# Kernel optimization log

Measured on AMD Instinct MI355X. Metric: run time of the kernel, lower is better.

## Reference

```python
import jax, jax.numpy as jnp
import numpy as np

B, L, D, H = 16, 1024, 1024, 16
HD = D // H  # head dim = 64


def setup_inputs() -> dict:
    rng = jax.random.key(0)
    ks = jax.random.split(rng, 12)
    s = 0.02
    return {
        "key": jax.random.normal(ks[0], (B, L, D), jnp.float32),
        "value": jax.random.normal(ks[1], (B, L, D), jnp.float32),
        "query": jax.random.normal(ks[2], (B, L, D), jnp.float32),
        "atten_masks": jax.random.randint(ks[3], (B, L, L), 0, 2, jnp.int32),
        "Wk": jax.random.normal(ks[4], (D, D), jnp.float32) * s,
        "bk": jnp.zeros((D,), jnp.float32),
        "Wq": jax.random.normal(ks[5], (D, D), jnp.float32) * s,
        "bq": jnp.zeros((D,), jnp.float32),
        "Wv": jax.random.normal(ks[6], (D, D), jnp.float32) * s,
        "bv": jnp.zeros((D,), jnp.float32),
        "Wp": jax.random.normal(ks[7], (D, D), jnp.float32) * s,
        "bp": jnp.zeros((D,), jnp.float32),
    }


def reference(key, value, query, atten_masks, Wk, bk, Wq, bq, Wv, bv, Wp, bp):
    # Linear projections (torch nn.Linear: x @ W^T + b)
    def lin(x, W, b):
        return x @ W.T + b

    # [B, L, D] -> [B, H, L, HD]
    def heads(x):
        return x.reshape(B, L, H, HD).transpose(0, 2, 1, 3)

    k = heads(lin(key, Wk, bk))
    q = heads(lin(query, Wq, bq))
    v = heads(lin(value, Wv, bv))

    scale = 1.0 / np.sqrt(HD).astype(np.float32)
    att = jnp.einsum("bhqd,bhkd->bhqk", q, k) * scale  # [B, H, L, L]
    att = jnp.where(atten_masks[:, None, :, :] == 0, -jnp.inf, att)
    att = jax.nn.softmax(att, axis=-1)

    y = jnp.einsum("bhqk,bhkd->bhqd", att, v)  # [B, H, L, HD]
    y = y.transpose(0, 2, 1, 3).reshape(B, L, D)
    return lin(y, Wp, bp)
```

## Files before the change

kernel.cpp:

```cpp
#include <hip/hip_runtime.h>

typedef __bf16 bf16_t;
typedef __bf16 bf16x4 __attribute__((ext_vector_type(4)));
typedef __bf16 bf16x8 __attribute__((ext_vector_type(8)));
typedef float f32x4 __attribute__((ext_vector_type(4)));
typedef float f32x16 __attribute__((ext_vector_type(16)));
typedef unsigned u32x2 __attribute__((ext_vector_type(2)));

#define QSCALE 0.18033688f

__device__ __forceinline__ int swz(int row) { return (row ^ (row >> 3)) & 7; }
__device__ __forceinline__ int swz2(int row) { return (row ^ (row >> 2)) & 3; }
__device__ __forceinline__ int swzv(int row) { return (row ^ (row >> 3)) & 15; }

__device__ __forceinline__ f32x4 mfma16(bf16x8 a, bf16x8 b, f32x4 c) {
  return __builtin_amdgcn_mfma_f32_16x16x32_bf16(a, b, c, 0, 0, 0);
}
__device__ __forceinline__ f32x16 mfma32(bf16x8 a, bf16x8 b, f32x16 c) {
  return __builtin_amdgcn_mfma_f32_32x32x16_bf16(a, b, c, 0, 0, 0);
}

__device__ __forceinline__ void gl_lds16(const void* g, void* l) {
  __builtin_amdgcn_global_load_lds(
      (const __attribute__((address_space(1))) unsigned int*)g,
      (__attribute__((address_space(3))) unsigned int*)l, 16, 0, 0);
}

__global__ __launch_bounds__(256) void cvt_all_kernel(
    const float* __restrict__ key, const float* __restrict__ query,
    const float* __restrict__ value, const float* __restrict__ Wk,
    const float* __restrict__ Wq, const float* __restrict__ Wv,
    const float* __restrict__ Wp, const int* __restrict__ mask,
    bf16_t* __restrict__ I1, bf16_t* __restrict__ I2, bf16_t* __restrict__ I3,
    bf16_t* __restrict__ Wkb, bf16_t* __restrict__ Wqb,
    bf16_t* __restrict__ Wvb, bf16_t* __restrict__ Wpb,
    unsigned* __restrict__ mbits) {
  const int bid = blockIdx.x;
  if (bid >= 53248) {
    int idx = (bid - 53248) * 256 + threadIdx.x;
    const int4* src = (const int4*)(mask + (size_t)idx * 32);
    unsigned w = 0;
#pragma unroll
    for (int i = 0; i < 8; ++i) {
      int4 v = src[i];
      w |= (v.x != 0 ? 1u : 0u) << (i * 4 + 0);
      w |= (v.y != 0 ? 1u : 0u) << (i * 4 + 1);
      w |= (v.z != 0 ? 1u : 0u) << (i * 4 + 2);
      w |= (v.w != 0 ? 1u : 0u) << (i * 4 + 3);
    }
    mbits[idx] = w;
    return;
  }
  const float* s;
  bf16_t* d;
  int base;
  float sc = 1.0f;
  if (bid < 16384) { s = key; d = I1; base = bid; }
  else if (bid < 32768) { s = query; d = I2; base = bid - 16384; }
  else if (bid < 49152) { s = value; d = I3; base = bid - 32768; }
  else if (bid < 50176) { s = Wk; d = Wkb; base = bid - 49152; }
  else if (bid < 51200) { s = Wq; d = Wqb; base = bid - 50176; sc = QSCALE; }
  else if (bid < 52224) { s = Wv; d = Wvb; base = bid - 51200; }
  else { s = Wp; d = Wpb; base = bid - 52224; }
  int i = base * 256 + threadIdx.x;
  float4 v = ((const float4*)s)[i];
  bf16x4 o;
  o[0] = (bf16_t)(v.x * sc); o[1] = (bf16_t)(v.y * sc);
  o[2] = (bf16_t)(v.z * sc); o[3] = (bf16_t)(v.w * sc);
  ((bf16x4*)d)[i] = o;
}

template <typename OT>
__device__ __forceinline__ void gemm256_body(const bf16_t* __restrict__ A,
                                             const bf16_t* __restrict__ W,
                                             const float* __restrict__ bias,
                                             float bscale,
                                             OT* __restrict__ O) {
  extern __shared__ __align__(16) char smem[];
  bf16_t* AsBase = (bf16_t*)smem;
  bf16_t* BsBase = (bf16_t*)(smem + 3 * 8192 * 2);

  const int t = threadIdx.x;
  const int lane = t & 63;
  const int wid = t >> 6;
  const int g = lane >> 4;
  const int lr = lane & 15;
  const int wm = wid >> 2, wn = wid & 3;
  const int lid = blockIdx.x;
  const int logical = (lid & 7) * 32 + (lid >> 3);
  const int m0 = (logical >> 2) * 256;
  const int n0 = (logical & 3) * 256;

  f32x4 acc[8][4] = {};

  auto STAGE_HALF = [&](int buf, int kb, int rr) {
    bf16_t* Ab = AsBase + buf * 8192;
    bf16_t* Bb = BsBase + buf * 8192;
    int s = rr * 512 + t;
    int row = s >> 2, c = s & 3;
    gl_lds16(A + (size_t)(m0 + row) * 1024 + kb + (c ^ swz2(row)) * 8,
             &Ab[(rr * 512 + wid * 64) * 8]);
    gl_lds16(W + (size_t)(n0 + row) * 1024 + kb + (c ^ swz2(row)) * 8,
             &Bb[(rr * 512 + wid * 64) * 8]);
  };

  STAGE_HALF(0, 0, 0);  STAGE_HALF(0, 0, 1);
  STAGE_HALF(1, 32, 0); STAGE_HALF(1, 32, 1);

  int cur = 0;
  for (int kb = 0; kb < 1024; kb += 32) {
    if (kb + 32 < 1024)
      asm volatile("s_waitcnt vmcnt(4)" ::: "memory");
    else
      asm volatile("s_waitcnt vmcnt(0)" ::: "memory");
    __builtin_amdgcn_sched_barrier(0);
    __builtin_amdgcn_s_barrier();
    __builtin_amdgcn_sched_barrier(0);

    const bool more = kb + 64 < 1024;
    int fut = cur + 2;
    if (fut >= 3) fut -= 3;
    const bf16_t* Ab = AsBase + cur * 8192;
    const bf16_t* Bb = BsBase + cur * 8192;

    if (more) STAGE_HALF(fut, kb + 64, 0);
    bf16x8 b[4], a0[4];
#pragma unroll
    for (int j = 0; j < 4; ++j) {
      int row = wn * 64 + j * 16 + lr;
      b[j] = *(const bf16x8*)&Bb[row * 32 + ((g ^ swz2(row))) * 8];
    }
#pragma unroll
    for (int i = 0; i < 4; ++i) {
      int row = wm * 128 + i * 16 + lr;
      a0[i] = *(const bf16x8*)&Ab[row * 32 + ((g ^ swz2(row))) * 8];
    }
    __builtin_amdgcn_s_setprio(1);
#pragma unroll
    for (int i = 0; i < 4; ++i)
#pragma unroll
      for (int j = 0; j < 4; ++j)
        acc[i][j] = mfma16(a0[i], b[j], acc[i][j]);
    __builtin_amdgcn_s_setprio(0);

    __builtin_amdgcn_sched_barrier(0);
    __builtin_amdgcn_s_barrier();
    __builtin_amdgcn_sched_barrier(0);

    if (more) STAGE_HALF(fut, kb + 64, 1);
    bf16x8 a1[4];
#pragma unroll
    for (int i = 0; i < 4; ++i) {
      int row = wm * 128 + (4 + i) * 16 + lr;
      a1[i] = *(const bf16x8*)&Ab[row * 32 + ((g ^ swz2(row))) * 8];
    }
    __builtin_amdgcn_s_setprio(1);
#pragma unroll
    for (int i = 0; i < 4; ++i)
#pragma unroll
      for (int j = 0; j < 4; ++j)
        acc[4 + i][j] = mfma16(a1[i], b[j], acc[4 + i][j]);
    __builtin_amdgcn_s_setprio(0);

    cur = cur + 1;
    if (cur >= 3) cur -= 3;
  }

  float bval[4];
#pragma unroll
  for (int j = 0; j < 4; ++j)
    bval[j] = bias[n0 + wn * 64 + j * 16 + lr] * bscale;
#pragma unroll
  for (int i = 0; i < 8; ++i)
#pragma unroll
    for (int r = 0; r < 4; ++r) {
      int row = m0 + wm * 128 + i * 16 + g * 4 + r;
#pragma unroll
      for (int j = 0; j < 4; ++j) {
        int n = n0 + wn * 64 + j * 16 + lr;
        O[(size_t)row * 1024 + n] = (OT)(acc[i][j][r] + bval[j]);
      }
    }
}

__global__ __launch_bounds__(512, 2) void gemm256_qkv_kernel(
    const bf16_t* key, const bf16_t* query, const bf16_t* value,
    const bf16_t* Wkb, const bf16_t* Wqb, const bf16_t* Wvb, const float* bk,
    const float* bq, const float* bv, bf16_t* ko, bf16_t* qo, bf16_t* vo) {
  const bf16_t *A, *W;
  const float* bi;
  bf16_t* O;
  float bs = 1.0f;
  if (blockIdx.y == 0) { A = key; W = Wkb; bi = bk; O = ko; }
  else if (blockIdx.y == 1) { A = query; W = Wqb; bi = bq; O = qo; bs = QSCALE; }
  else { A = value; W = Wvb; bi = bv; O = vo; }
  gemm256_body<bf16_t>(A, W, bi, bs, O);
}

__global__ __launch_bounds__(512, 2) void gemm256_out_kernel(
    const bf16_t* __restrict__ A, const bf16_t* __restrict__ W,
    const float* __restrict__ b, float* __restrict__ O) {
  gemm256_body<float>(A, W, b, 1.0f, O);
}

__global__ __launch_bounds__(256) void transpose_v_kernel(
    const bf16_t* __restrict__ v_ws, bf16_t* __restrict__ vT) {
  __shared__ bf16_t T[64 * 66];
  const int kc = blockIdx.x, h = blockIdx.y, b = blockIdx.z;
  const int t = threadIdx.x;
  {
    int key = t >> 2, dblk = t & 3;
    const bf16_t* src =
        v_ws + ((size_t)(b * 1024 + kc * 64 + key)) * 1024 + h * 64 + dblk * 16;
    bf16x8 a0 = *(const bf16x8*)src;
    bf16x8 a1 = *(const bf16x8*)(src + 8);
    bf16_t* row = &T[key * 66 + dblk * 16];
#pragma unroll
    for (int j = 0; j < 4; ++j) {
      ((unsigned*)row)[j] = ((const unsigned*)&a0)[j];
      ((unsigned*)row)[j + 4] = ((const unsigned*)&a1)[j];
    }
  }
  __syncthreads();
  {
    int d = t >> 2, kcl = t & 3;
    bf16x8 o0, o1;
#pragma unroll
    for (int e = 0; e < 8; ++e) {
      o0[e] = T[(kcl * 16 + e) * 66 + d];
      o1[e] = T[(kcl * 16 + 8 + e) * 66 + d];
    }
    bf16_t* dst =
        vT + ((size_t)((b * 16 + h) * 64 + d)) * 1024 + kc * 64 + kcl * 16;
    *(bf16x8*)dst = o0;
    *(bf16x8*)(dst + 8) = o1;
  }
}

__global__ __launch_bounds__(512) void attn_kernel(
    const bf16_t* __restrict__ q_ws, const bf16_t* __restrict__ k_ws,
    const bf16_t* __restrict__ vT, const unsigned* __restrict__ mbits,
    bf16_t* __restrict__ y_ws) {
  __shared__ __align__(16) bf16_t Ks[128 * 64];
  __shared__ __align__(16) bf16_t Vs[64 * 128];

  const int lid = blockIdx.x;
  const int logical = (lid & 7) * 128 + (lid >> 3);
  const int qb = logical & 3;
  const int h = (logical >> 2) & 15;
  const int b = logical >> 6;
  const int t = threadIdx.x, lane = t & 63, wid = t >> 6;
  const int ql = lane & 31;
  const int hh = lane >> 5;
  const int q = qb * 256 + wid * 32 + ql;

  bf16x8 qf[4];
  {
    const bf16_t* qp = q_ws + ((size_t)(b * 1024 + q)) * 1024 + h * 64 + hh * 8;
#pragma unroll
    for (int kc = 0; kc < 4; ++kc) qf[kc] = *(const bf16x8*)(qp + kc * 16);
  }

  bf16x8 onesf;
#pragma unroll
  for (int e = 0; e < 8; ++e) onesf[e] = (bf16_t)1.0f;

  f32x16 acc0 = {}, acc1 = {}, accl = {};
  const bf16_t* Kb = k_ws + ((size_t)b * 1024) * 1024 + h * 64;
  const bf16_t* Vb = vT + ((size_t)((b * 16 + h) * 64)) * 1024;
  const unsigned* mrow = mbits + ((size_t)(b * 1024 + q)) * 32;

  for (int kb = 0; kb < 8; ++kb) {
    __syncthreads();
#pragma unroll
    for (int rr = 0; rr < 2; ++rr) {
      int s = rr * 512 + t;
      int row = s >> 3, c = s & 7;
      gl_lds16(Kb + (size_t)(kb * 128 + row) * 1024 + (c ^ swz(row)) * 8,
               &Ks[(rr * 512 + wid * 64) * 8]);
    }
#pragma unroll
    for (int rr = 0; rr < 2; ++rr) {
      int s = rr * 512 + t;
      int row = s >> 4, c = s & 15;
      gl_lds16(Vb + (size_t)row * 1024 + kb * 128 + ((c ^ swzv(row))) * 8,
               &Vs[(rr * 512 + wid * 64) * 8]);
    }
    uint4 mw = *(const uint4*)&mrow[kb * 4];
    __syncthreads();

#pragma unroll
    for (int ct = 0; ct < 4; ++ct) {
      f32x16 c = {};
      __builtin_amdgcn_s_setprio(1);
#pragma unroll
      for (int kc = 0; kc < 4; ++kc) {
        int row = ct * 32 + ql;
        bf16x8 kf = *(const bf16x8*)&Ks[row * 64 + (((kc * 2 + hh) ^ swz(row))) * 8];
        c = mfma32(kf, qf[kc], c);
      }
      __builtin_amdgcn_s_setprio(0);

      unsigned w = ((const unsigned*)&mw)[ct] >> (4 * hh);
      float p[16];
#pragma unroll
      for (int r = 0; r < 16; ++r) {
        const int posr = (r & 3) + 8 * (r >> 2);
        int nm = (int)(w << (31 - posr)) >> 31;
        float e0 = __builtin_amdgcn_exp2f(c[r]);
        p[r] = __int_as_float(__float_as_int(e0) & nm);
      }

      bf16x8 pbt[2];
#pragma unroll
      for (int j = 0; j < 2; ++j) {
        const int base = j * 8;
        union { bf16_t h[2]; unsigned u; } a0, a1, b0, b1;
        a0.h[0] = (bf16_t)p[base + 0]; a0.h[1] = (bf16_t)p[base + 1];
        a1.h[0] = (bf16_t)p[base + 2]; a1.h[1] = (bf16_t)p[base + 3];
        b0.h[0] = (bf16_t)p[base + 4]; b0.h[1] = (bf16_t)p[base + 5];
        b1.h[0] = (bf16_t)p[base + 6]; b1.h[1] = (bf16_t)p[base + 7];
        u32x2 s0 = __builtin_amdgcn_permlane32_swap(a0.u, b0.u, false, false);
        u32x2 s1 = __builtin_amdgcn_permlane32_swap(a1.u, b1.u, false, false);
        union { unsigned u[4]; bf16x8 v; } pk;
        pk.u[0] = s0.x;
        pk.u[1] = s1.x;
        pk.u[2] = s0.y;
        pk.u[3] = s1.y;
        pbt[j] = pk.v;
      }

      __builtin_amdgcn_s_setprio(1);
#pragma unroll
      for (int j = 0; j < 2; ++j) {
        int sl = (2 * ct + j) * 2 + hh;
        {
          int row = ql;
          bf16x8 vf = *(const bf16x8*)&Vs[row * 128 + ((sl ^ swzv(row))) * 8];
          acc0 = mfma32(vf, pbt[j], acc0);
        }
        {
          int row = 32 + ql;
          bf16x8 vf = *(const bf16x8*)&Vs[row * 128 + ((sl ^ swzv(row))) * 8];
          acc1 = mfma32(vf, pbt[j], acc1);
        }
        accl = mfma32(onesf, pbt[j], accl);
      }
      __builtin_amdgcn_s_setprio(0);
    }
  }

  float inv = 1.0f / fmaxf(accl[0], 1e-30f);
  bf16_t* yp = y_ws + ((size_t)(b * 1024 + q)) * 1024 + h * 64;
#pragma unroll
  for (int j = 0; j < 4; ++j) {
    bf16x4 o0, o1;
#pragma unroll
    for (int e = 0; e < 4; ++e) {
      o0[e] = (bf16_t)(acc0[4 * j + e] * inv);
      o1[e] = (bf16_t)(acc1[4 * j + e] * inv);
    }
    *(bf16x4*)&yp[8 * j + 4 * hh] = o0;
    *(bf16x4*)&yp[32 + 8 * j + 4 * hh] = o1;
  }
}

extern "C" void kernel_launch(void* const* d_in, const int* in_sizes, int n_in,
                              void* d_out, int out_size, void* d_ws,
                              size_t ws_size, hipStream_t stream) {
  (void)in_sizes; (void)n_in; (void)out_size; (void)ws_size;
  const float* key = (const float*)d_in[0];
  const float* value = (const float*)d_in[1];
  const float* query = (const float*)d_in[2];
  const int* mask = (const int*)d_in[3];
  const float* Wk = (const float*)d_in[4];
  const float* bk = (const float*)d_in[5];
  const float* Wq = (const float*)d_in[6];
  const float* bq = (const float*)d_in[7];
  const float* Wv = (const float*)d_in[8];
  const float* bv = (const float*)d_in[9];
  const float* Wp = (const float*)d_in[10];
  const float* bp = (const float*)d_in[11];
  float* out = (float*)d_out;

  char* ws = (char*)d_ws;
  const size_t MB = 1ull << 20;
  unsigned* mbits = (unsigned*)(ws);
  bf16_t* Wkb = (bf16_t*)(ws + 2 * MB);
  bf16_t* Wqb = (bf16_t*)(ws + 4 * MB);
  bf16_t* Wvb = (bf16_t*)(ws + 6 * MB);
  bf16_t* Wpb = (bf16_t*)(ws + 8 * MB);
  bf16_t* I1 = (bf16_t*)(ws + 10 * MB);
  bf16_t* I2 = (bf16_t*)(ws + 42 * MB);
  bf16_t* I3 = (bf16_t*)(ws + 74 * MB);
  bf16_t* k_ws = (bf16_t*)(ws + 106 * MB);
  bf16_t* q_ws = (bf16_t*)(ws + 138 * MB);
  bf16_t* v_ws = (bf16_t*)(ws + 170 * MB);
  bf16_t* vT_ws = I1;
  bf16_t* y_ws = I2;

  const size_t GEMM_LDS = 3 * 8192 * 2 * 2;

  cvt_all_kernel<<<55296, 256, 0, stream>>>(key, query, value, Wk, Wq, Wv, Wp,
                                            mask, I1, I2, I3, Wkb, Wqb, Wvb,
                                            Wpb, mbits);
  gemm256_qkv_kernel<<<dim3(256, 3), 512, GEMM_LDS, stream>>>(
      I1, I2, I3, Wkb, Wqb, Wvb, bk, bq, bv, k_ws, q_ws, v_ws);
  transpose_v_kernel<<<dim3(16, 16, 16), 256, 0, stream>>>(v_ws, vT_ws);
  attn_kernel<<<1024, 512, 0, stream>>>(q_ws, k_ws, vT_ws, mbits, y_ws);
  gemm256_out_kernel<<<256, 512, GEMM_LDS, stream>>>(y_ws, Wpb, bp, out);
}
```

Measured before the change: 344.7 us.

## Shrink GEMM tile to 256x128 and merge half-stage pipeline into single stage

Changes the projection GEMM tile from 256x256 to 256x128, doubling the grid to 512 blocks per GEMM so more of the machine's CUs are occupied, with a smaller LDS footprint. The two half-step barriers per k-iteration are merged into one stage with a single barrier, and each wave now computes 8x2 MFMA tiles. The cost is lower arithmetic intensity: more global and LDS traffic per FLOP, since the A tile is reloaded by twice as many blocks.

```diff
diff --git a/kernel.cpp b/kernel.cpp
--- a/kernel.cpp
+++ b/kernel.cpp
@@ -87,97 +87,85 @@
   const int lr = lane & 15;
   const int wm = wid >> 2, wn = wid & 3;
   const int lid = blockIdx.x;
-  const int logical = (lid & 7) * 32 + (lid >> 3);
-  const int m0 = (logical >> 2) * 256;
-  const int n0 = (logical & 3) * 256;
-
-  f32x4 acc[8][4] = {};
-
-  auto STAGE_HALF = [&](int buf, int kb, int rr) {
+  const int logical = (lid & 7) * 64 + (lid >> 3);
+  const int m0 = (logical >> 3) * 256;
+  const int n0 = (logical & 7) * 128;
+
+  f32x4 acc[8][2] = {};
+
+  auto STAGE = [&](int buf, int kb) {
     bf16_t* Ab = AsBase + buf * 8192;
-    bf16_t* Bb = BsBase + buf * 8192;
-    int s = rr * 512 + t;
-    int row = s >> 2, c = s & 3;
-    gl_lds16(A + (size_t)(m0 + row) * 1024 + kb + (c ^ swz2(row)) * 8,
-             &Ab[(rr * 512 + wid * 64) * 8]);
-    gl_lds16(W + (size_t)(n0 + row) * 1024 + kb + (c ^ swz2(row)) * 8,
-             &Bb[(rr * 512 + wid * 64) * 8]);
+    bf16_t* Bb = BsBase + buf * 4096;
+#pragma unroll
+    for (int rr = 0; rr < 2; ++rr) {
+      int s = rr * 512 + t;
+      int row = s >> 2, c = s & 3;
+      gl_lds16(A + (size_t)(m0 + row) * 1024 + kb + (c ^ swz2(row)) * 8,
+               &Ab[(rr * 512 + wid * 64) * 8]);
+    }
+    {
+      int row = t >> 2, c = t & 3;
+      gl_lds16(W + (size_t)(n0 + row) * 1024 + kb + (c ^ swz2(row)) * 8,
+               &Bb[(wid * 64 + lane) * 8]);
+    }
   };
 
-  STAGE_HALF(0, 0, 0);  STAGE_HALF(0, 0, 1);
-  STAGE_HALF(1, 32, 0); STAGE_HALF(1, 32, 1);
+  STAGE(0, 0);
+  STAGE(1, 32);
 
   int cur = 0;
   for (int kb = 0; kb < 1024; kb += 32) {
     if (kb + 32 < 1024)
-      asm volatile("s_waitcnt vmcnt(4)" ::: "memory");
+      asm volatile("s_waitcnt vmcnt(3)" ::: "memory");
     else
       asm volatile("s_waitcnt vmcnt(0)" ::: "memory");
     __builtin_amdgcn_sched_barrier(0);
     __builtin_amdgcn_s_barrier();
     __builtin_amdgcn_sched_barrier(0);
 
-    const bool more = kb + 64 < 1024;
-    int fut = cur + 2;
-    if (fut >= 3) fut -= 3;
+    if (kb + 64 < 1024) {
+      int fut = cur + 2;
+      if (fut >= 3) fut -= 3;
+      STAGE(fut, kb + 64);
+    }
+
     const bf16_t* Ab = AsBase + cur * 8192;
-    const bf16_t* Bb = BsBase + cur * 8192;
-
-    if (more) STAGE_HALF(fut, kb + 64, 0);
-    bf16x8 b[4], a0[4];
-#pragma unroll
-    for (int j = 0; j < 4; ++j) {
-      int row = wn * 64 + j * 16 + lr;
+    const bf16_t* Bb = BsBase + cur * 4096;
+    bf16x8 a[8], b[2];
+#pragma unroll
+    for (int i = 0; i < 8; ++i) {
+      int row = wm * 128 + i * 16 + lr;
+      a[i] = *(const bf16x8*)&Ab[row * 32 + ((g ^ swz2(row))) * 8];
+    }
+#pragma unroll
+    for (int j = 0; j < 2; ++j) {
+      int row = wn * 32 + j * 16 + lr;
       b[j] = *(const bf16x8*)&Bb[row * 32 + ((g ^ swz2(row))) * 8];
     }
-#pragma unroll
-    for (int i = 0; i < 4; ++i) {
-      int row = wm * 128 + i * 16 + lr;
-      a0[i] = *(const bf16x8*)&Ab[row * 32 + ((g ^ swz2(row))) * 8];
-    }
     __builtin_amdgcn_s_setprio(1);
 #pragma unroll
-    for (int i = 0; i < 4; ++i)
-#pragma unroll
-      for (int j = 0; j < 4; ++j)
-        acc[i][j] = mfma16(a0[i], b[j], acc[i][j]);
-    __builtin_amdgcn_s_setprio(0);
-
-    __builtin_amdgcn_sched_barrier(0);
-    __builtin_amdgcn_s_barrier();
-    __builtin_amdgcn_sched_barrier(0);
-
-    if (more) STAGE_HALF(fut, kb + 64, 1);
-    bf16x8 a1[4];
-#pragma unroll
-    for (int i = 0; i < 4; ++i) {
-      int row = wm * 128 + (4 + i) * 16 + lr;
-      a1[i] = *(const bf16x8*)&Ab[row * 32 + ((g ^ swz2(row))) * 8];
-    }
-    __builtin_amdgcn_s_setprio(1);
-#pragma unroll
-    for (int i = 0; i < 4; ++i)
-#pragma unroll
-      for (int j = 0; j < 4; ++j)
-        acc[4 + i][j] = mfma16(a1[i], b[j], acc[4 + i][j]);
+    for (int i = 0; i < 8; ++i)
+#pragma unroll
+      for (int j = 0; j < 2; ++j)
+        acc[i][j] = mfma16(a[i], b[j], acc[i][j]);
     __builtin_amdgcn_s_setprio(0);
 
     cur = cur + 1;
     if (cur >= 3) cur -= 3;
   }
 
-  float bval[4];
-#pragma unroll
-  for (int j = 0; j < 4; ++j)
-    bval[j] = bias[n0 + wn * 64 + j * 16 + lr] * bscale;
+  float bval[2];
+#pragma unroll
+  for (int j = 0; j < 2; ++j)
+    bval[j] = bias[n0 + wn * 32 + j * 16 + lr] * bscale;
 #pragma unroll
   for (int i = 0; i < 8; ++i)
 #pragma unroll
     for (int r = 0; r < 4; ++r) {
       int row = m0 + wm * 128 + i * 16 + g * 4 + r;
 #pragma unroll
-      for (int j = 0; j < 4; ++j) {
-        int n = n0 + wn * 64 + j * 16 + lr;
+      for (int j = 0; j < 2; ++j) {
+        int n = n0 + wn * 32 + j * 16 + lr;
         O[(size_t)row * 1024 + n] = (OT)(acc[i][j][r] + bval[j]);
       }
     }
@@ -399,14 +387,14 @@
   bf16_t* vT_ws = I1;
   bf16_t* y_ws = I2;
 
-  const size_t GEMM_LDS = 3 * 8192 * 2 * 2;
+  const size_t GEMM_LDS = 3 * (8192 + 4096) * 2;
 
   cvt_all_kernel<<<55296, 256, 0, stream>>>(key, query, value, Wk, Wq, Wv, Wp,
                                             mask, I1, I2, I3, Wkb, Wqb, Wvb,
                                             Wpb, mbits);
-  gemm256_qkv_kernel<<<dim3(256, 3), 512, GEMM_LDS, stream>>>(
+  gemm256_qkv_kernel<<<dim3(512, 3), 512, GEMM_LDS, stream>>>(
       I1, I2, I3, Wkb, Wqb, Wvb, bk, bq, bv, k_ws, q_ws, v_ws);
   transpose_v_kernel<<<dim3(16, 16, 16), 256, 0, stream>>>(v_ws, vT_ws);
   attn_kernel<<<1024, 512, 0, stream>>>(q_ws, k_ws, vT_ws, mbits, y_ws);
-  gemm256_out_kernel<<<256, 512, GEMM_LDS, stream>>>(y_ws, Wpb, bp, out);
-}
+  gemm256_out_kernel<<<512, 512, GEMM_LDS, stream>>>(y_ws, Wpb, bp, out);
+}
```

Measured after the change: 348.3 us. Within noise of the previous version (+1.0%).
